# Performance work log

Measured on AMD Instinct MI355X. Metric: run time of the kernel, lower is better.

Reference implementation:

```python
import jax, jax.numpy as jnp
import numpy as np

EMBED = 1024
HEADS = 16
HEAD_DIM = EMBED // HEADS
WIN = 256  # attention_window w; band width = 2w+1


def setup_inputs() -> dict:
    key = jax.random.key(0)
    ks = jax.random.split(key, 10)
    b, s, e = 2, 4096, EMBED
    scale = 1.0 / np.sqrt(e)
    inp = {"x": jax.random.normal(ks[0], (b, s, e), jnp.float32)}
    for i, (wn, bn) in enumerate([("Wq", "bq"), ("Wk", "bk"), ("Wv", "bv"), ("Wo", "bo")]):
        inp[wn] = jax.random.normal(ks[1 + i], (e, e), jnp.float32) * scale
        inp[bn] = jax.random.normal(ks[5 + i], (e,), jnp.float32) * 0.01
    return inp


def _rope_headaxis(x):
    # Replicates RotaryEmbedding applied to [b, s, h, d]: the original indexes
    # x.shape[2] (== num_heads here), so phase varies over the HEAD axis.
    h, d = x.shape[2], x.shape[3]
    inv = 1.0 / (10000.0 ** (jnp.arange(0, d, 2, dtype=jnp.float32) / d))
    freqs = jnp.arange(h, dtype=jnp.float32)[:, None] * inv[None, :]
    emb = jnp.concatenate([freqs, freqs], axis=-1)  # [h, d]
    cos = jnp.cos(emb)[None, None]  # [1,1,h,d]
    sin = jnp.sin(emb)[None, None]
    x2 = jnp.stack([-x[..., 1::2], x[..., 0::2]], axis=-1).reshape(x.shape)
    return x * cos + x2 * sin


def reference(x, Wq, bq, Wk, bk, Wv, bv, Wo, bo):
    b, s, e = x.shape
    h, d, w = HEADS, HEAD_DIM, WIN
    q = (x @ Wq.T + bq).reshape(b, s, h, d)
    k = (x @ Wk.T + bk).reshape(b, s, h, d)
    v = (x @ Wv.T + bv).reshape(b, s, h, d)
    q = _rope_headaxis(q) / jnp.sqrt(jnp.float32(d))
    k = _rope_headaxis(k)

    # Band (sliding-window) attention: query chunk c of size w attends to key
    # chunks c-1, c, c+1 (3w keys); relative-position + boundary masking makes
    # this identical to the original sliding_chunks band of width 2w+1.
    nc = s // w
    qc = q.reshape(b, nc, w, h, d)
    pad = [(0, 0), (w, w), (0, 0), (0, 0)]
    kp = jnp.pad(k, pad)
    vp = jnp.pad(v, pad)
    idx = jnp.arange(nc)[:, None] * w + jnp.arange(3 * w)[None, :]  # [nc, 3w]
    k3 = kp[:, idx]  # [b, nc, 3w, h, d]
    v3 = vp[:, idx]
    scores = jnp.einsum('bcxhd,bcyhd->bhcxy', qc, k3)  # [b,h,nc,w,3w]

    c = jnp.arange(nc)[:, None, None]
    xq = jnp.arange(w)[None, :, None]
    y = jnp.arange(3 * w)[None, None, :]
    kpos = c * w + y - w  # absolute key position
    valid = (y >= xq) & (y <= xq + 2 * w) & (kpos >= 0) & (kpos < s)
    scores = jnp.where(valid[None, None], scores, -jnp.inf)

    probs = jax.nn.softmax(scores, axis=-1)  # fp32 softmax, as in original
    ctx = jnp.einsum('bhcxy,bcyhd->bcxhd', probs, v3).reshape(b, s, e)
    return ctx @ Wo.T + bo
```

## Files before the change

### kernel.cpp

```cpp
#include <hip/hip_runtime.h>


typedef _Float16 half8 __attribute__((ext_vector_type(8)));
typedef _Float16 half4v __attribute__((ext_vector_type(4)));
typedef float floatx4 __attribute__((ext_vector_type(4)));

typedef __attribute__((address_space(3))) unsigned int lds_u32;
typedef const __attribute__((address_space(1))) unsigned int glb_u32;

__device__ __forceinline__ void async_copy16(const void* g, void* l) {
  __builtin_amdgcn_global_load_lds((glb_u32*)g, (lds_u32*)l, 16, 0, 0);
}

__global__ __launch_bounds__(256) void convert_kernel(
    const float* __restrict__ x, const float* __restrict__ wq,
    const float* __restrict__ wk, const float* __restrict__ wv,
    const float* __restrict__ wo, _Float16* __restrict__ dst) {
  const int e0 = (blockIdx.x * 256 + threadIdx.x) * 4;
  const float* src; int off;
  if      (e0 <  8388608) { src = x;  off = e0; }
  else if (e0 <  9437184) { src = wq; off = e0 -  8388608; }
  else if (e0 < 10485760) { src = wk; off = e0 -  9437184; }
  else if (e0 < 11534336) { src = wv; off = e0 - 10485760; }
  else                    { src = wo; off = e0 - 11534336; }
  const float4 f = *(const float4*)(src + off);
  half4v h;
  h[0] = (_Float16)f.x; h[1] = (_Float16)f.y;
  h[2] = (_Float16)f.z; h[3] = (_Float16)f.w;
  *(half4v*)(dst + e0) = h;
}

__global__ __launch_bounds__(256, 4) void gemm_qkv_kernel(
    const _Float16* __restrict__ A, const _Float16* __restrict__ w0,
    const _Float16* __restrict__ w1, const _Float16* __restrict__ w2,
    const float* __restrict__ b0, const float* __restrict__ b1,
    const float* __restrict__ b2, _Float16* __restrict__ o0,
    _Float16* __restrict__ o1, _Float16* __restrict__ o2) {
  __shared__ _Float16 smem[17408];
  _Float16* As = smem;
  _Float16* Bs = smem + 8192;

  const int tid = threadIdx.x;
  const int w = tid >> 6, lane = tid & 63;
  const int l4 = lane & 15, quad = lane >> 4;
  const int wm = w & 1, wn = w >> 1;

  const int bid = blockIdx.x;
  const int xcd = bid & 7, li = bid >> 3;
  const int z = li >> 6, r_ = li & 63;
  const int n_l = r_ >> 3, m_l = r_ & 7;
  const int m0 = (xcd * 8 + m_l) * 128;
  const int n0 = n_l * 128;

  const _Float16* B; const float* bias; _Float16* out;
  if (z == 0)      { B = w0; bias = b0; out = o0; }
  else if (z == 1) { B = w1; bias = b1; out = o1; }
  else             { B = w2; bias = b2; out = o2; }
  const bool dorope = z < 2;
  const float scl = (z == 0) ? 0.18033688f : 1.0f;

  const floatx4 zero = {0.f, 0.f, 0.f, 0.f};
  floatx4 acc[4][4];
#pragma unroll
  for (int i = 0; i < 4; ++i)
#pragma unroll
    for (int j = 0; j < 4; ++j) acc[i][j] = zero;

  for (int kt = 0; kt < 16; ++kt) {
    const int k0 = kt * 64;
#pragma unroll
    for (int i = 0; i < 4; ++i) {
      const int p = i * 256 + tid;
      const int r = p >> 3;
      const int c = (p & 7) ^ (r & 7);
      async_copy16(A + (m0 + r) * 1024 + k0 + c * 8, As + (i * 256 + w * 64) * 8);
      async_copy16(B + (n0 + r) * 1024 + k0 + c * 8, Bs + (i * 256 + w * 64) * 8);
    }
    __syncthreads();
#pragma unroll
    for (int ks = 0; ks < 2; ++ks) {
      half8 af[4], bf[4];
#pragma unroll
      for (int mt = 0; mt < 4; ++mt)
        af[mt] = *(const half8*)(As + (wm * 64 + mt * 16 + l4) * 64 +
                                 (((ks * 4 + quad) ^ (l4 & 7)) * 8));
#pragma unroll
      for (int nt = 0; nt < 4; ++nt)
        bf[nt] = *(const half8*)(Bs + (wn * 64 + nt * 16 + l4) * 64 +
                                 (((ks * 4 + quad) ^ (l4 & 7)) * 8));
#pragma unroll
      for (int mt = 0; mt < 4; ++mt)
#pragma unroll
        for (int nt = 0; nt < 4; ++nt)
          acc[mt][nt] = __builtin_amdgcn_mfma_f32_16x16x32_f16(af[mt], bf[nt], acc[mt][nt], 0, 0, 0);
    }
    __syncthreads();
  }

  _Float16* tile = smem;
#pragma unroll
  for (int nt = 0; nt < 4; ++nt) {
    const int n = n0 + wn * 64 + nt * 16 + l4;
    const float bval = bias[n];
    const int hh = n >> 6;
    float c_ = 1.f, ss = 0.f;
    if (dorope) {
      const float freq = __expf((float)(n & 31) * -0.28782314f);
      float s_;
      __sincosf((float)hh * freq, &s_, &c_);
      ss = (n & 1) ? s_ : -s_;
    }
#pragma unroll
    for (int mt = 0; mt < 4; ++mt)
#pragma unroll
      for (int r = 0; r < 4; ++r) {
        float val = acc[mt][nt][r] + bval;
        const float prt = __shfl_xor(val, 1);
        if (dorope) val = (val * c_ + prt * ss) * scl;
        const int ml = wm * 64 + mt * 16 + quad * 4 + r;
        const int nl = wn * 64 + nt * 16 + l4;
        if (z == 2) tile[nl * 132 + ml] = (_Float16)val;
        else        tile[ml * 132 + nl] = (_Float16)val;
      }
  }
  __syncthreads();
  if (z == 2) {
#pragma unroll
    for (int j = 0; j < 8; ++j) {
      const int idx = j * 256 + tid;
      const int row = idx >> 4, cb = idx & 15;
      const int n = n0 + row, hh = n >> 6, dd = n & 63;
      const int m = m0 + cb * 8, bb = m >> 12, s = m & 4095;
      const half8 vals = *(const half8*)(tile + row * 132 + cb * 8);
      *(half8*)(out + (bb * 16 + hh) * 262144 + dd * 4096 + s) = vals;
    }
  } else {
#pragma unroll
    for (int j = 0; j < 8; ++j) {
      const int idx = j * 256 + tid;
      const int row = idx >> 4, cb = idx & 15;
      const int n = n0 + cb * 8, hh = n >> 6, dd = n & 63;
      const int m = m0 + row, bb = m >> 12, s = m & 4095;
      const half8 vals = *(const half8*)(tile + row * 132 + cb * 8);
      *(half8*)(out + ((bb * 16 + hh) * 4096 + s) * 64 + dd) = vals;
    }
  }
}

__global__ __launch_bounds__(256, 4) void gemm_out_kernel(
    const _Float16* __restrict__ A, const _Float16* __restrict__ B,
    const float* __restrict__ bias, float* __restrict__ out) {
  __shared__ _Float16 smem[16384];
  _Float16* As = smem;
  _Float16* Bs = smem + 8192;

  const int tid = threadIdx.x;
  const int w = tid >> 6, lane = tid & 63;
  const int l4 = lane & 15, quad = lane >> 4;
  const int wm = w & 1, wn = w >> 1;

  const int bid = blockIdx.x;
  const int xcd = bid & 7, li = bid >> 3;
  const int n_l = li >> 3, m_l = li & 7;
  const int m0 = (xcd * 8 + m_l) * 128;
  const int n0 = n_l * 128;

  const floatx4 zero = {0.f, 0.f, 0.f, 0.f};
  floatx4 acc[4][4];
#pragma unroll
  for (int i = 0; i < 4; ++i)
#pragma unroll
    for (int j = 0; j < 4; ++j) acc[i][j] = zero;

  for (int kt = 0; kt < 16; ++kt) {
    const int k0 = kt * 64;
#pragma unroll
    for (int i = 0; i < 4; ++i) {
      const int p = i * 256 + tid;
      const int r = p >> 3;
      const int c = (p & 7) ^ (r & 7);
      async_copy16(A + (m0 + r) * 1024 + k0 + c * 8, As + (i * 256 + w * 64) * 8);
      async_copy16(B + (n0 + r) * 1024 + k0 + c * 8, Bs + (i * 256 + w * 64) * 8);
    }
    __syncthreads();
#pragma unroll
    for (int ks = 0; ks < 2; ++ks) {
      half8 af[4], bf[4];
#pragma unroll
      for (int mt = 0; mt < 4; ++mt)
        af[mt] = *(const half8*)(As + (wm * 64 + mt * 16 + l4) * 64 +
                                 (((ks * 4 + quad) ^ (l4 & 7)) * 8));
#pragma unroll
      for (int nt = 0; nt < 4; ++nt)
        bf[nt] = *(const half8*)(Bs + (wn * 64 + nt * 16 + l4) * 64 +
                                 (((ks * 4 + quad) ^ (l4 & 7)) * 8));
#pragma unroll
      for (int mt = 0; mt < 4; ++mt)
#pragma unroll
        for (int nt = 0; nt < 4; ++nt)
          acc[mt][nt] = __builtin_amdgcn_mfma_f32_16x16x32_f16(af[mt], bf[nt], acc[mt][nt], 0, 0, 0);
    }
    __syncthreads();
  }

#pragma unroll
  for (int nt = 0; nt < 4; ++nt) {
    const int n = n0 + wn * 64 + nt * 16 + l4;
    const float bval = bias[n];
#pragma unroll
    for (int mt = 0; mt < 4; ++mt)
#pragma unroll
      for (int r = 0; r < 4; ++r) {
        const int m = m0 + wm * 64 + mt * 16 + quad * 4 + r;
        out[m * 1024 + n] = acc[mt][nt][r] + bval;
      }
  }
}

__global__ __launch_bounds__(256, 4) void attn_kernel(
    const _Float16* __restrict__ qg, const _Float16* __restrict__ kg,
    const _Float16* __restrict__ vtg, _Float16* __restrict__ ctx) {
  __shared__ _Float16 Ks[128 * 64];
  __shared__ _Float16 Vs[64 * 128];

  const int tid = threadIdx.x;
  const int w = tid >> 6, lane = tid & 63;
  const int l4 = lane & 15, quad = lane >> 4;
  const int q0 = blockIdx.x * 128;
  const int bh = blockIdx.y;
  const _Float16* qbh = qg + bh * 262144;
  const _Float16* kbh = kg + bh * 262144;
  const _Float16* vbh = vtg + bh * 262144;

  half8 qf[2][2];
#pragma unroll
  for (int nt = 0; nt < 2; ++nt)
#pragma unroll
    for (int ks = 0; ks < 2; ++ks)
      qf[nt][ks] = *(const half8*)(qbh + (q0 + w * 32 + nt * 16 + l4) * 64 + ks * 32 + quad * 8);

  const floatx4 zero = {0.f, 0.f, 0.f, 0.f};
  floatx4 OT[4][2];
  float m_st[2], l_st[2];
#pragma unroll
  for (int md = 0; md < 4; ++md)
#pragma unroll
    for (int nt = 0; nt < 2; ++nt) OT[md][nt] = zero;
#pragma unroll
  for (int nt = 0; nt < 2; ++nt) { m_st[nt] = -1e30f; l_st[nt] = 0.f; }

  for (int t = 0; t < 5; ++t) {
    const int kv0 = q0 + (t - 2) * 128;
    if (kv0 < 0 || kv0 >= 4096) continue;

#pragma unroll
    for (int i = 0; i < 4; ++i) {
      const int p = i * 256 + tid;
      const int rk = p >> 3, ck = (p & 7) ^ (rk & 7);
      async_copy16(kbh + (kv0 + rk) * 64 + ck * 8, Ks + (i * 256 + w * 64) * 8);
      const int rv = p >> 4, cv = (p & 15) ^ (rv & 7);
      async_copy16(vbh + rv * 4096 + kv0 + cv * 8, Vs + (i * 256 + w * 64) * 8);
    }
    __syncthreads();

    const bool edge = (t == 0 || t == 4);
#pragma unroll
    for (int hf = 0; hf < 2; ++hf) {
      const int kb = hf * 64;

      floatx4 ST[4][2];
#pragma unroll
      for (int m = 0; m < 4; ++m)
#pragma unroll
        for (int nt = 0; nt < 2; ++nt) ST[m][nt] = zero;
#pragma unroll
      for (int ks = 0; ks < 2; ++ks)
#pragma unroll
        for (int m = 0; m < 4; ++m) {
          const half8 kf = *(const half8*)(Ks + (kb + m * 16 + l4) * 64 +
                                           ((ks * 4 + quad) ^ (l4 & 7)) * 8);
#pragma unroll
          for (int nt = 0; nt < 2; ++nt)
            ST[m][nt] = __builtin_amdgcn_mfma_f32_16x16x32_f16(kf, qf[nt][ks], ST[m][nt], 0, 0, 0);
        }

      if (edge) {
#pragma unroll
        for (int m = 0; m < 4; ++m)
#pragma unroll
          for (int r = 0; r < 4; ++r) {
            const int key = kv0 + kb + m * 16 + quad * 4 + r;
#pragma unroll
            for (int nt = 0; nt < 2; ++nt) {
              const int d = key - (q0 + w * 32 + nt * 16 + l4);
              if (d < -256 || d > 256) ST[m][nt][r] = -1e30f;
            }
          }
      }

#pragma unroll
      for (int nt = 0; nt < 2; ++nt) {
        float mx = -1e30f;
#pragma unroll
        for (int m = 0; m < 4; ++m)
#pragma unroll
          for (int r = 0; r < 4; ++r) mx = fmaxf(mx, ST[m][nt][r]);
        mx = fmaxf(mx, __shfl_xor(mx, 16));
        mx = fmaxf(mx, __shfl_xor(mx, 32));
        const float mnew = fmaxf(m_st[nt], mx);
        const float alpha = exp2f(m_st[nt] - mnew);
        m_st[nt] = mnew;
        float rs = 0.f;
#pragma unroll
        for (int m = 0; m < 4; ++m)
#pragma unroll
          for (int r = 0; r < 4; ++r) {
            const float pv = exp2f(ST[m][nt][r] - mnew);
            ST[m][nt][r] = pv;
            rs += pv;
          }
        rs += __shfl_xor(rs, 16);
        rs += __shfl_xor(rs, 32);
        l_st[nt] = l_st[nt] * alpha + rs;
#pragma unroll
        for (int md = 0; md < 4; ++md)
#pragma unroll
          for (int r = 0; r < 4; ++r) OT[md][nt][r] *= alpha;
      }

#pragma unroll
      for (int m = 0; m < 4; ++m) {
        half4v pb[2];
#pragma unroll
        for (int nt = 0; nt < 2; ++nt) {
          const auto lo = __builtin_amdgcn_cvt_pkrtz(ST[m][nt][0], ST[m][nt][1]);
          const auto hi = __builtin_amdgcn_cvt_pkrtz(ST[m][nt][2], ST[m][nt][3]);
          pb[nt][0] = (_Float16)lo[0]; pb[nt][1] = (_Float16)lo[1];
          pb[nt][2] = (_Float16)hi[0]; pb[nt][3] = (_Float16)hi[1];
        }
#pragma unroll
        for (int md = 0; md < 4; ++md) {
          const half4v vf = *(const half4v*)(Vs + (md * 16 + l4) * 128 +
                                             (((hf * 8 + m * 2 + (quad >> 1)) ^ (l4 & 7)) * 8 +
                                              (quad & 1) * 4));
#pragma unroll
          for (int nt = 0; nt < 2; ++nt)
            OT[md][nt] = __builtin_amdgcn_mfma_f32_16x16x16f16(vf, pb[nt], OT[md][nt], 0, 0, 0);
        }
      }
    }
    __syncthreads();
  }

  const int b = bh >> 4, hh = bh & 15;
#pragma unroll
  for (int nt = 0; nt < 2; ++nt) {
    const float inv_l = 1.f / l_st[nt];
    const int s = q0 + w * 32 + nt * 16 + l4;
#pragma unroll
    for (int md = 0; md < 4; ++md) {
      half4v o;
#pragma unroll
      for (int r = 0; r < 4; ++r) o[r] = (_Float16)(OT[md][nt][r] * inv_l);
      *(half4v*)(ctx + (b * 4096 + s) * 1024 + hh * 64 + md * 16 + quad * 4) = o;
    }
  }
}

extern "C" void kernel_launch(void* const* d_in, const int* in_sizes, int n_in,
                              void* d_out, int out_size, void* d_ws, size_t ws_size,
                              hipStream_t stream) {
  const float* x  = (const float*)d_in[0];
  const float* Wq = (const float*)d_in[1];
  const float* bq = (const float*)d_in[2];
  const float* Wk = (const float*)d_in[3];
  const float* bk = (const float*)d_in[4];
  const float* Wv = (const float*)d_in[5];
  const float* bv = (const float*)d_in[6];
  const float* Wo = (const float*)d_in[7];
  const float* bo = (const float*)d_in[8];

  _Float16* ws   = (_Float16*)d_ws;
  _Float16* xh   = ws;
  _Float16* wqh  = ws + 8388608;
  _Float16* wkh  = ws + 9437184;
  _Float16* wvh  = ws + 10485760;
  _Float16* woh  = ws + 11534336;
  _Float16* qh   = ws + 12582912;
  _Float16* kh   = ws + 20971520;
  _Float16* vth  = ws + 29360128;
  _Float16* ctxh = xh;

  convert_kernel<<<12288, 256, 0, stream>>>(x, Wq, Wk, Wv, Wo, ws);
  gemm_qkv_kernel<<<1536, 256, 0, stream>>>(xh, wqh, wkh, wvh,
                                            bq, bk, bv, qh, kh, vth);
  attn_kernel<<<dim3(32, 32), 256, 0, stream>>>(qh, kh, vth, ctxh);
  gemm_out_kernel<<<512, 256, 0, stream>>>(ctxh, woh, bo, (float*)d_out);
}
```

Baseline: 271.9 us.

## Process two query tiles per attention block to reuse loaded K/V tiles

```diff
diff --git a/kernel.cpp b/kernel.cpp
--- a/kernel.cpp
+++ b/kernel.cpp
@@ -30,7 +30,7 @@
   *(half4v*)(dst + e0) = h;
 }
 
-__global__ __launch_bounds__(256, 4) void gemm_qkv_kernel(
+__global__ __launch_bounds__(256, 2) void gemm_qkv_kernel(
     const _Float16* __restrict__ A, const _Float16* __restrict__ w0,
     const _Float16* __restrict__ w1, const _Float16* __restrict__ w2,
     const float* __restrict__ b0, const float* __restrict__ b1,
@@ -147,7 +147,7 @@
   }
 }
 
-__global__ __launch_bounds__(256, 4) void gemm_out_kernel(
+__global__ __launch_bounds__(256, 2) void gemm_out_kernel(
     const _Float16* __restrict__ A, const _Float16* __restrict__ B,
     const float* __restrict__ bias, float* __restrict__ out) {
   __shared__ _Float16 smem[16384];
@@ -217,7 +217,7 @@
   }
 }
 
-__global__ __launch_bounds__(256, 4) void attn_kernel(
+__global__ __launch_bounds__(256, 2) void attn_kernel(
     const _Float16* __restrict__ qg, const _Float16* __restrict__ kg,
     const _Float16* __restrict__ vtg, _Float16* __restrict__ ctx) {
   __shared__ _Float16 Ks[128 * 64];
@@ -226,31 +226,37 @@
   const int tid = threadIdx.x;
   const int w = tid >> 6, lane = tid & 63;
   const int l4 = lane & 15, quad = lane >> 4;
-  const int q0 = blockIdx.x * 128;
+  const int q0 = blockIdx.x * 256;
   const int bh = blockIdx.y;
   const _Float16* qbh = qg + bh * 262144;
   const _Float16* kbh = kg + bh * 262144;
   const _Float16* vbh = vtg + bh * 262144;
 
-  half8 qf[2][2];
-#pragma unroll
-  for (int nt = 0; nt < 2; ++nt)
-#pragma unroll
-    for (int ks = 0; ks < 2; ++ks)
-      qf[nt][ks] = *(const half8*)(qbh + (q0 + w * 32 + nt * 16 + l4) * 64 + ks * 32 + quad * 8);
+  half8 qf[2][2][2];
+#pragma unroll
+  for (int sub = 0; sub < 2; ++sub)
+#pragma unroll
+    for (int nt = 0; nt < 2; ++nt)
+#pragma unroll
+      for (int ks = 0; ks < 2; ++ks)
+        qf[sub][nt][ks] = *(const half8*)(qbh + (q0 + sub * 128 + w * 32 + nt * 16 + l4) * 64 +
+                                          ks * 32 + quad * 8);
 
   const floatx4 zero = {0.f, 0.f, 0.f, 0.f};
-  floatx4 OT[4][2];
-  float m_st[2], l_st[2];
-#pragma unroll
-  for (int md = 0; md < 4; ++md)
-#pragma unroll
-    for (int nt = 0; nt < 2; ++nt) OT[md][nt] = zero;
-#pragma unroll
-  for (int nt = 0; nt < 2; ++nt) { m_st[nt] = -1e30f; l_st[nt] = 0.f; }
-
-  for (int t = 0; t < 5; ++t) {
-    const int kv0 = q0 + (t - 2) * 128;
+  floatx4 OT[2][4][2];
+  float m_st[2][2], l_st[2][2];
+#pragma unroll
+  for (int sub = 0; sub < 2; ++sub) {
+#pragma unroll
+    for (int md = 0; md < 4; ++md)
+#pragma unroll
+      for (int nt = 0; nt < 2; ++nt) OT[sub][md][nt] = zero;
+#pragma unroll
+    for (int nt = 0; nt < 2; ++nt) { m_st[sub][nt] = -1e30f; l_st[sub][nt] = 0.f; }
+  }
+
+  for (int t = 0; t < 6; ++t) {
+    const int kv0 = q0 - 256 + t * 128;
     if (kv0 < 0 || kv0 >= 4096) continue;
 
 #pragma unroll
@@ -263,89 +269,93 @@
     }
     __syncthreads();
 
-    const bool edge = (t == 0 || t == 4);
-#pragma unroll
-    for (int hf = 0; hf < 2; ++hf) {
-      const int kb = hf * 64;
-
-      floatx4 ST[4][2];
-#pragma unroll
-      for (int m = 0; m < 4; ++m)
-#pragma unroll
-        for (int nt = 0; nt < 2; ++nt) ST[m][nt] = zero;
-#pragma unroll
-      for (int ks = 0; ks < 2; ++ks)
+    const bool edge = (t <= 1 || t >= 4);
+#pragma unroll
+    for (int sub = 0; sub < 2; ++sub) {
+      const int qbase = q0 + sub * 128 + w * 32;
+#pragma unroll
+      for (int hf = 0; hf < 2; ++hf) {
+        const int kb = hf * 64;
+
+        floatx4 ST[4][2];
+#pragma unroll
+        for (int m = 0; m < 4; ++m)
+#pragma unroll
+          for (int nt = 0; nt < 2; ++nt) ST[m][nt] = zero;
+#pragma unroll
+        for (int ks = 0; ks < 2; ++ks)
+#pragma unroll
+          for (int m = 0; m < 4; ++m) {
+            const half8 kf = *(const half8*)(Ks + (kb + m * 16 + l4) * 64 +
+                                             ((ks * 4 + quad) ^ (l4 & 7)) * 8);
+#pragma unroll
+            for (int nt = 0; nt < 2; ++nt)
+              ST[m][nt] = __builtin_amdgcn_mfma_f32_16x16x32_f16(kf, qf[sub][nt][ks], ST[m][nt], 0, 0, 0);
+          }
+
+        if (edge) {
+#pragma unroll
+          for (int m = 0; m < 4; ++m)
+#pragma unroll
+            for (int r = 0; r < 4; ++r) {
+              const int key = kv0 + kb + m * 16 + quad * 4 + r;
+#pragma unroll
+              for (int nt = 0; nt < 2; ++nt) {
+                const int d = key - (qbase + nt * 16 + l4);
+                if (d < -256 || d > 256) ST[m][nt][r] = -1e30f;
+              }
+            }
+        }
+
+#pragma unroll
+        for (int nt = 0; nt < 2; ++nt) {
+          float mx = -1e30f;
+#pragma unroll
+          for (int m = 0; m < 4; ++m)
+#pragma unroll
+            for (int r = 0; r < 4; ++r) mx = fmaxf(mx, ST[m][nt][r]);
+          mx = fmaxf(mx, __shfl_xor(mx, 16));
+          mx = fmaxf(mx, __shfl_xor(mx, 32));
+          const float mnew = fmaxf(m_st[sub][nt], mx);
+          const float alpha = exp2f(m_st[sub][nt] - mnew);
+          m_st[sub][nt] = mnew;
+          float rs = 0.f;
+#pragma unroll
+          for (int m = 0; m < 4; ++m)
+#pragma unroll
+            for (int r = 0; r < 4; ++r) {
+              const float pv = exp2f(ST[m][nt][r] - mnew);
+              ST[m][nt][r] = pv;
+              rs += pv;
+            }
+          rs += __shfl_xor(rs, 16);
+          rs += __shfl_xor(rs, 32);
+          l_st[sub][nt] = l_st[sub][nt] * alpha + rs;
+#pragma unroll
+          for (int md = 0; md < 4; ++md)
+#pragma unroll
+            for (int r = 0; r < 4; ++r) OT[sub][md][nt][r] *= alpha;
+        }
+
 #pragma unroll
         for (int m = 0; m < 4; ++m) {
-          const half8 kf = *(const half8*)(Ks + (kb + m * 16 + l4) * 64 +
-                                           ((ks * 4 + quad) ^ (l4 & 7)) * 8);
-#pragma unroll
-          for (int nt = 0; nt < 2; ++nt)
-            ST[m][nt] = __builtin_amdgcn_mfma_f32_16x16x32_f16(kf, qf[nt][ks], ST[m][nt], 0, 0, 0);
-        }
-
-      if (edge) {
-#pragma unroll
-        for (int m = 0; m < 4; ++m)
-#pragma unroll
-          for (int r = 0; r < 4; ++r) {
-            const int key = kv0 + kb + m * 16 + quad * 4 + r;
-#pragma unroll
-            for (int nt = 0; nt < 2; ++nt) {
-              const int d = key - (q0 + w * 32 + nt * 16 + l4);
-              if (d < -256 || d > 256) ST[m][nt][r] = -1e30f;
-            }
+          half4v pb[2];
+#pragma unroll
+          for (int nt = 0; nt < 2; ++nt) {
+            const auto lo = __builtin_amdgcn_cvt_pkrtz(ST[m][nt][0], ST[m][nt][1]);
+            const auto hi = __builtin_amdgcn_cvt_pkrtz(ST[m][nt][2], ST[m][nt][3]);
+            pb[nt][0] = (_Float16)lo[0]; pb[nt][1] = (_Float16)lo[1];
+            pb[nt][2] = (_Float16)hi[0]; pb[nt][3] = (_Float16)hi[1];
           }
-      }
-
-#pragma unroll
-      for (int nt = 0; nt < 2; ++nt) {
-        float mx = -1e30f;
-#pragma unroll
-        for (int m = 0; m < 4; ++m)
-#pragma unroll
-          for (int r = 0; r < 4; ++r) mx = fmaxf(mx, ST[m][nt][r]);
-        mx = fmaxf(mx, __shfl_xor(mx, 16));
-        mx = fmaxf(mx, __shfl_xor(mx, 32));
-        const float mnew = fmaxf(m_st[nt], mx);
-        const float alpha = exp2f(m_st[nt] - mnew);
-        m_st[nt] = mnew;
-        float rs = 0.f;
-#pragma unroll
-        for (int m = 0; m < 4; ++m)
-#pragma unroll
-          for (int r = 0; r < 4; ++r) {
-            const float pv = exp2f(ST[m][nt][r] - mnew);
-            ST[m][nt][r] = pv;
-            rs += pv;
+#pragma unroll
+          for (int md = 0; md < 4; ++md) {
+            const half4v vf = *(const half4v*)(Vs + (md * 16 + l4) * 128 +
+                                               (((hf * 8 + m * 2 + (quad >> 1)) ^ (l4 & 7)) * 8 +
+                                                (quad & 1) * 4));
+#pragma unroll
+            for (int nt = 0; nt < 2; ++nt)
+              OT[sub][md][nt] = __builtin_amdgcn_mfma_f32_16x16x16f16(vf, pb[nt], OT[sub][md][nt], 0, 0, 0);
           }
-        rs += __shfl_xor(rs, 16);
-        rs += __shfl_xor(rs, 32);
-        l_st[nt] = l_st[nt] * alpha + rs;
-#pragma unroll
-        for (int md = 0; md < 4; ++md)
-#pragma unroll
-          for (int r = 0; r < 4; ++r) OT[md][nt][r] *= alpha;
-      }
-
-#pragma unroll
-      for (int m = 0; m < 4; ++m) {
-        half4v pb[2];
-#pragma unroll
-        for (int nt = 0; nt < 2; ++nt) {
-          const auto lo = __builtin_amdgcn_cvt_pkrtz(ST[m][nt][0], ST[m][nt][1]);
-          const auto hi = __builtin_amdgcn_cvt_pkrtz(ST[m][nt][2], ST[m][nt][3]);
-          pb[nt][0] = (_Float16)lo[0]; pb[nt][1] = (_Float16)lo[1];
-          pb[nt][2] = (_Float16)hi[0]; pb[nt][3] = (_Float16)hi[1];
-        }
-#pragma unroll
-        for (int md = 0; md < 4; ++md) {
-          const half4v vf = *(const half4v*)(Vs + (md * 16 + l4) * 128 +
-                                             (((hf * 8 + m * 2 + (quad >> 1)) ^ (l4 & 7)) * 8 +
-                                              (quad & 1) * 4));
-#pragma unroll
-          for (int nt = 0; nt < 2; ++nt)
-            OT[md][nt] = __builtin_amdgcn_mfma_f32_16x16x16f16(vf, pb[nt], OT[md][nt], 0, 0, 0);
         }
       }
     }
@@ -354,17 +364,19 @@
 
   const int b = bh >> 4, hh = bh & 15;
 #pragma unroll
-  for (int nt = 0; nt < 2; ++nt) {
-    const float inv_l = 1.f / l_st[nt];
-    const int s = q0 + w * 32 + nt * 16 + l4;
-#pragma unroll
-    for (int md = 0; md < 4; ++md) {
-      half4v o;
-#pragma unroll
-      for (int r = 0; r < 4; ++r) o[r] = (_Float16)(OT[md][nt][r] * inv_l);
-      *(half4v*)(ctx + (b * 4096 + s) * 1024 + hh * 64 + md * 16 + quad * 4) = o;
-    }
-  }
+  for (int sub = 0; sub < 2; ++sub)
+#pragma unroll
+    for (int nt = 0; nt < 2; ++nt) {
+      const float inv_l = 1.f / l_st[sub][nt];
+      const int s = q0 + sub * 128 + w * 32 + nt * 16 + l4;
+#pragma unroll
+      for (int md = 0; md < 4; ++md) {
+        half4v o;
+#pragma unroll
+        for (int r = 0; r < 4; ++r) o[r] = (_Float16)(OT[sub][md][nt][r] * inv_l);
+        *(half4v*)(ctx + (b * 4096 + s) * 1024 + hh * 64 + md * 16 + quad * 4) = o;
+      }
+    }
 }
 
 extern "C" void kernel_launch(void* const* d_in, const int* in_sizes, int n_in,
@@ -394,6 +406,6 @@
   convert_kernel<<<12288, 256, 0, stream>>>(x, Wq, Wk, Wv, Wo, ws);
   gemm_qkv_kernel<<<1536, 256, 0, stream>>>(xh, wqh, wkh, wvh,
                                             bq, bk, bv, qh, kh, vth);
-  attn_kernel<<<dim3(32, 32), 256, 0, stream>>>(qh, kh, vth, ctxh);
+  attn_kernel<<<dim3(16, 32), 256, 0, stream>>>(qh, kh, vth, ctxh);
   gemm_out_kernel<<<512, 256, 0, stream>>>(ctxh, woh, bo, (float*)d_out);
 }
```

Result: faster. 259.0 us (-4.7%).
